# Kernel tuning notes

Measured on AMD Instinct MI355X. Metric: run time of the kernel, lower is better.

## Reference

```python
import jax, jax.numpy as jnp
import numpy as np

HIDDEN = 256
INPUT = 256
OUTPUT = 256
BATCH = 256
SEQ = 512


def setup_inputs() -> dict:
    key = jax.random.key(0)
    ks = jax.random.split(key, 9)
    d = INPUT + HIDDEN
    s = 0.05
    return {
        "x": jax.random.normal(ks[0], (BATCH, SEQ, INPUT), dtype=jnp.float32),
        "Wr": jax.random.normal(ks[1], (d, HIDDEN), dtype=jnp.float32) * s,
        "br": jax.random.normal(ks[2], (HIDDEN,), dtype=jnp.float32) * s,
        "Wz": jax.random.normal(ks[3], (d, HIDDEN), dtype=jnp.float32) * s,
        "bz": jax.random.normal(ks[4], (HIDDEN,), dtype=jnp.float32) * s,
        "Wh": jax.random.normal(ks[5], (d, HIDDEN), dtype=jnp.float32) * s,
        "bh": jax.random.normal(ks[6], (HIDDEN,), dtype=jnp.float32) * s,
        "Wo": jax.random.normal(ks[7], (HIDDEN, OUTPUT), dtype=jnp.float32) * s,
        "bo": jax.random.normal(ks[8], (OUTPUT,), dtype=jnp.float32) * s,
    }


def reference(x, Wr, br, Wz, bz, Wh, bh, Wo, bo):
    # x: [B, S, I]. Sequential GRU cell; only last-step output is returned
    # (the torch loop overwrites `output` each iteration).
    B = x.shape[0]
    h0 = jnp.zeros((B, HIDDEN), dtype=x.dtype)

    def step(h, xt):
        combined = jnp.concatenate([xt, h], axis=1)          # [B, I+H]
        r = jax.nn.sigmoid(combined @ Wr + br)                # reset gate
        z = jax.nn.sigmoid(combined @ Wz + bz)                # update gate
        combined2 = jnp.concatenate([xt, r * h], axis=1)
        h_cand = jnp.tanh(combined2 @ Wh + bh)
        h_new = z * h + (1.0 - z) * h_cand
        return h_new, None

    xs = jnp.swapaxes(x, 0, 1)  # [S, B, I] for scan over time
    h_last, _ = jax.lax.scan(step, h0, xs)
    return h_last @ Wo + bo
```

## Files before the change

kernel.cpp:

```cpp
#include <hip/hip_runtime.h>
#include <math.h>


#define BATCH  256
#define SEQ    512
#define INPUT  256
#define HIDDEN 256
#define DTOT   512
#define NTC    48
#define NT_O   16
#define LOG2E  1.44269504088896f

typedef float          f32x4 __attribute__((ext_vector_type(4)));
typedef short          s16x8 __attribute__((ext_vector_type(8)));
typedef unsigned short u16x8 __attribute__((ext_vector_type(8)));
typedef unsigned int   u32x2 __attribute__((ext_vector_type(2)));

#define WH_OFF   0u
#define WX_OFF   393216u
#define WO_OFF   786432u
#define X_OFF    917504u
#define WS_NEED     (917504ull + 201326592ull)
#define WS_NEED_OLD 786432ull

__device__ __forceinline__ unsigned short f2bf(float f) {
    unsigned int u = __float_as_uint(f);
    u += 0x7FFFu + ((u >> 16) & 1u);
    return (unsigned short)(u >> 16);
}
__device__ __forceinline__ unsigned short f2bf_fast(float f) {
    return (unsigned short)((__float_as_uint(f) + 0x8000u) >> 16);
}
__device__ __forceinline__ float bf2f(unsigned short u) {
    return __uint_as_float(((unsigned int)u) << 16);
}
__device__ __forceinline__ f32x4 cvt4(u32x2 u) {
    f32x4 a;
    a[0] = __uint_as_float(u[0] << 16);
    a[1] = __uint_as_float(u[0] & 0xffff0000u);
    a[2] = __uint_as_float(u[1] << 16);
    a[3] = __uint_as_float(u[1] & 0xffff0000u);
    return a;
}
__device__ __forceinline__ unsigned int pk2bf(float a, float b) {
    return ((__float_as_uint(a) + 0x8000u) >> 16) |
           ((__float_as_uint(b) + 0x8000u) & 0xFFFF0000u);
}
#if __has_builtin(__builtin_amdgcn_exp2f)
#define EXP2F(x) __builtin_amdgcn_exp2f(x)
#else
#define EXP2F(x) exp2f(x)
#endif
#if __has_builtin(__builtin_amdgcn_rcpf)
#define RCPF(x) __builtin_amdgcn_rcpf(x)
#else
#define RCPF(x) (1.0f / (x))
#endif

#define WAITCNT_VM3()   asm volatile("s_waitcnt vmcnt(3)" ::: "memory")
#define WAITCNT_VM4()   asm volatile("s_waitcnt vmcnt(4)" ::: "memory")
#define WAITCNT_LGKM0() asm volatile("s_waitcnt lgkmcnt(0)" ::: "memory")
#define BAR() do { __builtin_amdgcn_s_barrier(); __builtin_amdgcn_sched_barrier(0); } while (0)

__device__ __forceinline__ void async_ld16(const void* g, void* l) {
    __builtin_amdgcn_global_load_lds(
        (const __attribute__((address_space(1))) unsigned int*)g,
        (__attribute__((address_space(3))) unsigned int*)l, 16, 0, 0);
}

__device__ __forceinline__ void ntc_decode(int ntc, int& gate, int& colbase) {
    int w = ntc / 6, s = ntc - 6 * w;
    gate = s >> 1;
    colbase = (2 * w + (s & 1)) * 16;
}

__global__ __launch_bounds__(256) void pack_weights_k(
    const float* __restrict__ Wr, const float* __restrict__ Wz,
    const float* __restrict__ Wh, const float* __restrict__ Wo,
    unsigned short* __restrict__ ws)
{
    int tid = blockIdx.x * 256 + threadIdx.x;
    int tile = tid >> 6;
    int l = tid & 63, quad = l >> 4, lan = l & 15;
    u16x8 v;
    unsigned short* dst;
    if (tile < 768) {
        int isH = tile < 384;
        int t2 = isH ? tile : tile - 384;
        int ntc = t2 >> 3, kt = t2 & 7;
        int gate, colbase;
        ntc_decode(ntc, gate, colbase);
        const float* W = gate == 0 ? Wr : (gate == 1 ? Wz : Wh);
        float scale = (gate == 2) ? 2.f * LOG2E : LOG2E;
        int col = colbase + lan;
        int kbase = (isH ? 256 : 0) + kt * 32 + quad * 8;
        #pragma unroll
        for (int j = 0; j < 8; ++j) v[j] = f2bf(W[(kbase + j) * 256 + col] * scale);
        dst = (unsigned short*)((char*)ws + (isH ? WH_OFF : WX_OFF)) + (size_t)(t2 * 64 + l) * 8;
    } else {
        int t2 = tile - 768;
        int kt = t2 / NT_O, nt = t2 % NT_O;
        int col = nt * 16 + lan;
        int kbase = kt * 32 + quad * 8;
        #pragma unroll
        for (int j = 0; j < 8; ++j) v[j] = f2bf(Wo[(kbase + j) * 256 + col]);
        dst = (unsigned short*)((char*)ws + WO_OFF) + (size_t)(t2 * 64 + l) * 8;
    }
    *(u16x8*)dst = v;
}

__global__ __launch_bounds__(256, 1) void xgemm_k(
    const float* __restrict__ x,
    const float* __restrict__ br, const float* __restrict__ bz, const float* __restrict__ bh,
    unsigned short* __restrict__ ws)
{
    __shared__ __align__(16) float Xf[2][16][260];
    const int th = threadIdx.x, wave = th >> 6, l = th & 63, quad = l >> 4, lan = l & 15;
    const s16x8* WX = (const s16x8*)((char*)ws + WX_OFF);
    s16x8 wx[12][8];
    #pragma unroll
    for (int fi = 0; fi < 12; ++fi)
        #pragma unroll
        for (int kt = 0; kt < 8; ++kt)
            wx[fi][kt] = WX[(((size_t)(12 * wave + fi)) * 8 + kt) * 64 + l];
    float bias[12];
    #pragma unroll
    for (int fi = 0; fi < 12; ++fi) {
        int gate, colbase;
        ntc_decode(12 * wave + fi, gate, colbase);
        const float* bb = gate == 0 ? br : (gate == 1 ? bz : bh);
        bias[fi] = bb[colbase + lan] * (gate == 2 ? 2.f * LOG2E : LOG2E);
    }
    u32x2* Xout = (u32x2*)((char*)ws + X_OFF);

    {
        int unit = blockIdx.x * 32, t = unit >> 4, gg = unit & 15;
        #pragma unroll
        for (int rr = 0; rr < 4; ++rr) {
            int row = rr * 4 + wave;
            const float* src = x + (((size_t)(gg * 16 + row)) * SEQ + t) * INPUT + l * 4;
            async_ld16(src, &Xf[0][row][0]);
        }
    }
    for (int uu = 0; uu < 32; ++uu) {
        BAR();
        if (uu + 1 < 32) {
            int unit = blockIdx.x * 32 + uu + 1, t = unit >> 4, gg = unit & 15;
            int nb = (uu + 1) & 1;
            #pragma unroll
            for (int rr = 0; rr < 4; ++rr) {
                int row = rr * 4 + wave;
                const float* src = x + (((size_t)(gg * 16 + row)) * SEQ + t) * INPUT + l * 4;
                async_ld16(src, &Xf[nb][row][0]);
            }
        }
        WAITCNT_VM4();
        BAR();
        int buf = uu & 1;
        f32x4 acc[12];
        #pragma unroll
        for (int fi = 0; fi < 12; ++fi) { acc[fi][0] = bias[fi]; acc[fi][1] = bias[fi]; acc[fi][2] = bias[fi]; acc[fi][3] = bias[fi]; }
        #pragma unroll
        for (int kt = 0; kt < 8; ++kt) {
            f32x4 a0 = *(const f32x4*)&Xf[buf][lan][kt * 32 + quad * 8];
            f32x4 a1 = *(const f32x4*)&Xf[buf][lan][kt * 32 + quad * 8 + 4];
            u16x8 ap;
            ap[0] = f2bf_fast(a0[0]); ap[1] = f2bf_fast(a0[1]); ap[2] = f2bf_fast(a0[2]); ap[3] = f2bf_fast(a0[3]);
            ap[4] = f2bf_fast(a1[0]); ap[5] = f2bf_fast(a1[1]); ap[6] = f2bf_fast(a1[2]); ap[7] = f2bf_fast(a1[3]);
            s16x8 a = (s16x8)ap;
            #pragma unroll
            for (int fi = 0; fi < 12; ++fi)
                acc[fi] = __builtin_amdgcn_mfma_f32_16x16x32_bf16(a, wx[fi][kt], acc[fi], 0, 0, 0);
        }
        size_t unit = (size_t)blockIdx.x * 32 + uu;
        #pragma unroll
        for (int fi = 0; fi < 12; ++fi) {
            u32x2 p;
            p[0] = pk2bf(acc[fi][0], acc[fi][1]);
            p[1] = pk2bf(acc[fi][2], acc[fi][3]);
            Xout[(unit * NTC + 12 * wave + fi) * 64 + l] = p;
        }
    }
}

__global__ __launch_bounds__(512, 2) void gru_rec_k(
    const float* __restrict__ bo,
    unsigned short* __restrict__ ws,
    float* __restrict__ out)
{
    extern __shared__ __align__(16) char smem[];
    unsigned short (*Hb)[264]  = (unsigned short (*)[264])smem;
    unsigned short (*RHb)[264] = (unsigned short (*)[264])(smem + 8448);
    char* Xr = smem + 16896;

    const int th = threadIdx.x, wave = th >> 6, l = th & 63, quad = l >> 4, lan = l & 15;
    const int b = blockIdx.x;
    const s16x8* WH = (const s16x8*)((char*)ws + WH_OFF);
    s16x8 wfr[2][8], wfz[2][8], wfc[2][8];
    #pragma unroll
    for (int i = 0; i < 2; ++i)
        #pragma unroll
        for (int kt = 0; kt < 8; ++kt) {
            wfr[i][kt] = WH[((6 * wave + i) * 8 + kt) * 64 + l];
            wfz[i][kt] = WH[((6 * wave + 2 + i) * 8 + kt) * 64 + l];
            wfc[i][kt] = WH[((6 * wave + 4 + i) * 8 + kt) * 64 + l];
        }
    for (int idx = th; idx < 16 * 264; idx += 512) ((unsigned short*)Hb)[idx] = 0;
    float h[2][4];
    #pragma unroll
    for (int i = 0; i < 2; ++i)
        #pragma unroll
        for (int r = 0; r < 4; ++r) h[i][r] = 0.f;

    const char* Xg = (const char*)ws + X_OFF;
    {
        const char* sb = Xg + (((size_t)b) * NTC + 6 * wave) * 512;
        char* db = Xr + wave * 3072;
        #pragma unroll
        for (int inst = 0; inst < 3; ++inst)
            async_ld16(sb + inst * 1024 + l * 16, db + inst * 1024);
    }
    __syncthreads();

    for (int t = 0; t < SEQ; ++t) {
        int buf = t & 1;
        {
            int t1 = (t + 1 < SEQ) ? t + 1 : t;
            const char* sb = Xg + (((size_t)(t1 * 16 + b)) * NTC + 6 * wave) * 512;
            char* db = Xr + (buf ^ 1) * 24576 + wave * 3072;
            #pragma unroll
            for (int inst = 0; inst < 3; ++inst)
                async_ld16(sb + inst * 1024 + l * 16, db + inst * 1024);
        }
        WAITCNT_VM3();
        const char* Xw = Xr + buf * 24576 + wave * 3072;

        f32x4 ar[2], az[2];
        #pragma unroll
        for (int i = 0; i < 2; ++i) {
            ar[i] = cvt4(*(const u32x2*)(Xw + (size_t)i * 512 + l * 8));
            az[i] = cvt4(*(const u32x2*)(Xw + (size_t)(2 + i) * 512 + l * 8));
        }
        #pragma unroll
        for (int kt = 0; kt < 8; ++kt) {
            s16x8 a = *(const s16x8*)&Hb[lan][kt * 32 + quad * 8];
            #pragma unroll
            for (int i = 0; i < 2; ++i) {
                ar[i] = __builtin_amdgcn_mfma_f32_16x16x32_bf16(a, wfr[i][kt], ar[i], 0, 0, 0);
                az[i] = __builtin_amdgcn_mfma_f32_16x16x32_bf16(a, wfz[i][kt], az[i], 0, 0, 0);
            }
        }
        #pragma unroll
        for (int i = 0; i < 2; ++i) {
            int col = (2 * wave + i) * 16 + lan;
            #pragma unroll
            for (int r = 0; r < 4; ++r) {
                float rg = RCPF(1.f + EXP2F(-ar[i][r]));
                RHb[quad * 4 + r][col] = f2bf_fast(rg * h[i][r]);
            }
        }
        WAITCNT_LGKM0();
        BAR();

        float zg[2][4];
        #pragma unroll
        for (int i = 0; i < 2; ++i)
            #pragma unroll
            for (int r = 0; r < 4; ++r)
                zg[i][r] = RCPF(1.f + EXP2F(-az[i][r]));

        f32x4 ac[2];
        #pragma unroll
        for (int i = 0; i < 2; ++i)
            ac[i] = cvt4(*(const u32x2*)(Xw + (size_t)(4 + i) * 512 + l * 8));
        #pragma unroll
        for (int kt = 0; kt < 8; ++kt) {
            s16x8 a = *(const s16x8*)&RHb[lan][kt * 32 + quad * 8];
            #pragma unroll
            for (int i = 0; i < 2; ++i)
                ac[i] = __builtin_amdgcn_mfma_f32_16x16x32_bf16(a, wfc[i][kt], ac[i], 0, 0, 0);
        }
        #pragma unroll
        for (int i = 0; i < 2; ++i) {
            int col = (2 * wave + i) * 16 + lan;
            #pragma unroll
            for (int r = 0; r < 4; ++r) {
                float e  = EXP2F(ac[i][r]);
                float hc = (e - 1.f) * RCPF(e + 1.f);
                float hn = zg[i][r] * (h[i][r] - hc) + hc;
                h[i][r] = hn;
                Hb[quad * 4 + r][col] = f2bf_fast(hn);
            }
        }
        WAITCNT_LGKM0();
        BAR();
    }

    const s16x8* WO = (const s16x8*)((char*)ws + WO_OFF);
    #pragma unroll
    for (int i = 0; i < 2; ++i) {
        int nt = 2 * wave + i;
        int col = nt * 16 + lan;
        float bv = bo[col];
        f32x4 acc;
        acc[0] = bv; acc[1] = bv; acc[2] = bv; acc[3] = bv;
        #pragma unroll
        for (int kt = 0; kt < 8; ++kt) {
            s16x8 a = *(const s16x8*)&Hb[lan][kt * 32 + quad * 8];
            acc = __builtin_amdgcn_mfma_f32_16x16x32_bf16(a, WO[(kt * NT_O + nt) * 64 + l], acc, 0, 0, 0);
        }
        #pragma unroll
        for (int r = 0; r < 4; ++r)
            out[(size_t)(b * 16 + quad * 4 + r) * 256 + col] = acc[r];
    }
}

__global__ __launch_bounds__(256) void prep_weights_k(
    const float* __restrict__ Wr, const float* __restrict__ Wz,
    const float* __restrict__ Wh, unsigned short* __restrict__ W16)
{
    const int n = DTOT * HIDDEN;
    int idx = blockIdx.x * 256 + threadIdx.x;
    if (idx >= 3 * n) return;
    int m = idx / n;
    int r = idx - m * n;
    const float* src = (m == 0) ? Wr : ((m == 1) ? Wz : Wh);
    W16[idx] = f2bf(src[r]);
}
__device__ __forceinline__ float ldw(const unsigned short* p) { return bf2f(*p); }
__device__ __forceinline__ float ldw(const float* p)          { return *p; }

template <typename WT>
__global__ __launch_bounds__(256) void gru_seq_k(
    const float* __restrict__ x,
    const WT* __restrict__ Wr, const WT* __restrict__ Wz, const WT* __restrict__ Wh,
    const float* __restrict__ br, const float* __restrict__ bz, const float* __restrict__ bh,
    const float* __restrict__ Wo, const float* __restrict__ bo,
    float* __restrict__ out)
{
    const int b = blockIdx.x, j = threadIdx.x;
    __shared__ float xh[DTOT];
    __shared__ float xrh[DTOT];
    xh[INPUT + j] = 0.0f;
    const float brj = br[j], bzj = bz[j], bhj = bh[j];
    const float* xb = x + (size_t)b * SEQ * INPUT;
    const WT* wrj = Wr + j;
    const WT* wzj = Wz + j;
    const WT* whj = Wh + j;
    __syncthreads();
    for (int t = 0; t < SEQ; ++t) {
        float xv = xb[t * INPUT + j];
        xh[j] = xv; xrh[j] = xv;
        __syncthreads();
        float ar = brj, az = bzj;
        #pragma unroll 8
        for (int k = 0; k < DTOT; ++k) {
            float v = xh[k];
            ar += v * ldw(wrj + k * HIDDEN);
            az += v * ldw(wzj + k * HIDDEN);
        }
        float rg = 1.0f / (1.0f + __expf(-ar));
        float zg = 1.0f / (1.0f + __expf(-az));
        float hj = xh[INPUT + j];
        xrh[INPUT + j] = rg * hj;
        __syncthreads();
        float ah = bhj;
        #pragma unroll 8
        for (int k = 0; k < DTOT; ++k) ah += xrh[k] * ldw(whj + k * HIDDEN);
        float hc = tanhf(ah);
        float hn = zg * hj + (1.0f - zg) * hc;
        xh[INPUT + j] = hn;
        __syncthreads();
    }
    float acc = bo[j];
    #pragma unroll 8
    for (int k = 0; k < HIDDEN; ++k) acc += xh[INPUT + k] * Wo[k * HIDDEN + j];
    out[(size_t)b * HIDDEN + j] = acc;
}

extern "C" void kernel_launch(void* const* d_in, const int* in_sizes, int n_in,
                              void* d_out, int out_size, void* d_ws, size_t ws_size,
                              hipStream_t stream) {
    const float* x  = (const float*)d_in[0];
    const float* Wr = (const float*)d_in[1];
    const float* br = (const float*)d_in[2];
    const float* Wz = (const float*)d_in[3];
    const float* bz = (const float*)d_in[4];
    const float* Wh = (const float*)d_in[5];
    const float* bh = (const float*)d_in[6];
    const float* Wo = (const float*)d_in[7];
    const float* bo = (const float*)d_in[8];
    float* out = (float*)d_out;

    if (ws_size >= WS_NEED) {
        unsigned short* ws = (unsigned short*)d_ws;
        (void)hipFuncSetAttribute((const void*)gru_rec_k,
                                  hipFuncAttributeMaxDynamicSharedMemorySize, 66048);
        pack_weights_k<<<224, 256, 0, stream>>>(Wr, Wz, Wh, Wo, ws);
        xgemm_k<<<256, 256, 0, stream>>>(x, br, bz, bh, ws);
        gru_rec_k<<<16, 512, 66048, stream>>>(bo, ws, out);
    } else if (ws_size >= WS_NEED_OLD) {
        unsigned short* W16 = (unsigned short*)d_ws;
        const size_t n = (size_t)DTOT * HIDDEN;
        prep_weights_k<<<(int)((3 * n + 255) / 256), 256, 0, stream>>>(Wr, Wz, Wh, W16);
        gru_seq_k<unsigned short><<<BATCH, 256, 0, stream>>>(
            x, W16, W16 + n, W16 + 2 * n, br, bz, bh, Wo, bo, out);
    } else {
        gru_seq_k<float><<<BATCH, 256, 0, stream>>>(
            x, Wr, Wz, Wh, br, bz, bh, Wo, bo, out);
    }
}
```

Measured before the change: 1.056 ms.

## Prefetch precomputed input projections into registers and split candidate MFMA chain

```diff
diff --git a/kernel.cpp b/kernel.cpp
--- a/kernel.cpp
+++ b/kernel.cpp
@@ -13,6 +13,7 @@
 
 typedef float          f32x4 __attribute__((ext_vector_type(4)));
 typedef short          s16x8 __attribute__((ext_vector_type(8)));
+typedef short          s16x4 __attribute__((ext_vector_type(4)));
 typedef unsigned short u16x8 __attribute__((ext_vector_type(8)));
 typedef unsigned int   u32x2 __attribute__((ext_vector_type(2)));
 
@@ -57,7 +58,6 @@
 #define RCPF(x) (1.0f / (x))
 #endif
 
-#define WAITCNT_VM3()   asm volatile("s_waitcnt vmcnt(3)" ::: "memory")
 #define WAITCNT_VM4()   asm volatile("s_waitcnt vmcnt(4)" ::: "memory")
 #define WAITCNT_LGKM0() asm volatile("s_waitcnt lgkmcnt(0)" ::: "memory")
 #define BAR() do { __builtin_amdgcn_s_barrier(); __builtin_amdgcn_sched_barrier(0); } while (0)
@@ -66,6 +66,12 @@
     __builtin_amdgcn_global_load_lds(
         (const __attribute__((address_space(1))) unsigned int*)g,
         (__attribute__((address_space(3))) unsigned int*)l, 16, 0, 0);
+}
+
+__device__ __forceinline__ s16x8 ld_frag(const unsigned short* row, int off) {
+    s16x4 lo = *(const s16x4*)(row + off);
+    s16x4 hi = *(const s16x4*)(row + off + 4);
+    return __builtin_shufflevector(lo, hi, 0, 1, 2, 3, 4, 5, 6, 7);
 }
 
 __device__ __forceinline__ void ntc_decode(int ntc, int& gate, int& colbase) {
@@ -188,10 +194,8 @@
     unsigned short* __restrict__ ws,
     float* __restrict__ out)
 {
-    extern __shared__ __align__(16) char smem[];
-    unsigned short (*Hb)[264]  = (unsigned short (*)[264])smem;
-    unsigned short (*RHb)[264] = (unsigned short (*)[264])(smem + 8448);
-    char* Xr = smem + 16896;
+    __shared__ __align__(16) unsigned short Hb[16][260];
+    __shared__ __align__(16) unsigned short RHb[16][260];
 
     const int th = threadIdx.x, wave = th >> 6, l = th & 63, quad = l >> 4, lan = l & 15;
     const int b = blockIdx.x;
@@ -205,45 +209,40 @@
             wfz[i][kt] = WH[((6 * wave + 2 + i) * 8 + kt) * 64 + l];
             wfc[i][kt] = WH[((6 * wave + 4 + i) * 8 + kt) * 64 + l];
         }
-    for (int idx = th; idx < 16 * 264; idx += 512) ((unsigned short*)Hb)[idx] = 0;
+    for (int idx = th; idx < 16 * 260; idx += 512) ((unsigned short*)Hb)[idx] = 0;
     float h[2][4];
     #pragma unroll
     for (int i = 0; i < 2; ++i)
         #pragma unroll
         for (int r = 0; r < 4; ++r) h[i][r] = 0.f;
 
-    const char* Xg = (const char*)ws + X_OFF;
-    {
-        const char* sb = Xg + (((size_t)b) * NTC + 6 * wave) * 512;
-        char* db = Xr + wave * 3072;
-        #pragma unroll
-        for (int inst = 0; inst < 3; ++inst)
-            async_ld16(sb + inst * 1024 + l * 16, db + inst * 1024);
-    }
+    const char* xp = (const char*)ws + X_OFF
+                   + (((size_t)b) * NTC + 6 * wave) * 512 + (size_t)l * 8;
+    const size_t XSTEP = (size_t)16 * NTC * 512;
+    u32x2 xn[6];
+    #pragma unroll
+    for (int j = 0; j < 6; ++j) xn[j] = *(const u32x2*)(xp + j * 512);
+
     __syncthreads();
 
     for (int t = 0; t < SEQ; ++t) {
-        int buf = t & 1;
-        {
-            int t1 = (t + 1 < SEQ) ? t + 1 : t;
-            const char* sb = Xg + (((size_t)(t1 * 16 + b)) * NTC + 6 * wave) * 512;
-            char* db = Xr + (buf ^ 1) * 24576 + wave * 3072;
-            #pragma unroll
-            for (int inst = 0; inst < 3; ++inst)
-                async_ld16(sb + inst * 1024 + l * 16, db + inst * 1024);
-        }
-        WAITCNT_VM3();
-        const char* Xw = Xr + buf * 24576 + wave * 3072;
+        u32x2 xc[6];
+        #pragma unroll
+        for (int j = 0; j < 6; ++j) xc[j] = xn[j];
+        if (t + 1 < SEQ) xp += XSTEP;
+        #pragma unroll
+        for (int j = 0; j < 6; ++j) xn[j] = *(const u32x2*)(xp + j * 512);
 
         f32x4 ar[2], az[2];
         #pragma unroll
         for (int i = 0; i < 2; ++i) {
-            ar[i] = cvt4(*(const u32x2*)(Xw + (size_t)i * 512 + l * 8));
-            az[i] = cvt4(*(const u32x2*)(Xw + (size_t)(2 + i) * 512 + l * 8));
-        }
+            ar[i] = cvt4(xc[i]);
+            az[i] = cvt4(xc[2 + i]);
+        }
+        const unsigned short* hrow = &Hb[lan][0];
         #pragma unroll
         for (int kt = 0; kt < 8; ++kt) {
-            s16x8 a = *(const s16x8*)&Hb[lan][kt * 32 + quad * 8];
+            s16x8 a = ld_frag(hrow, kt * 32 + quad * 8);
             #pragma unroll
             for (int i = 0; i < 2; ++i) {
                 ar[i] = __builtin_amdgcn_mfma_f32_16x16x32_bf16(a, wfr[i][kt], ar[i], 0, 0, 0);
@@ -269,23 +268,33 @@
             for (int r = 0; r < 4; ++r)
                 zg[i][r] = RCPF(1.f + EXP2F(-az[i][r]));
 
-        f32x4 ac[2];
-        #pragma unroll
-        for (int i = 0; i < 2; ++i)
-            ac[i] = cvt4(*(const u32x2*)(Xw + (size_t)(4 + i) * 512 + l * 8));
-        #pragma unroll
-        for (int kt = 0; kt < 8; ++kt) {
-            s16x8 a = *(const s16x8*)&RHb[lan][kt * 32 + quad * 8];
+        f32x4 acL[2], acH[2];
+        #pragma unroll
+        for (int i = 0; i < 2; ++i) {
+            acL[i] = cvt4(xc[4 + i]);
+            acH[i][0] = 0.f; acH[i][1] = 0.f; acH[i][2] = 0.f; acH[i][3] = 0.f;
+        }
+        const unsigned short* rrow = &RHb[lan][0];
+        #pragma unroll
+        for (int kt = 0; kt < 4; ++kt) {
+            s16x8 a = ld_frag(rrow, kt * 32 + quad * 8);
             #pragma unroll
             for (int i = 0; i < 2; ++i)
-                ac[i] = __builtin_amdgcn_mfma_f32_16x16x32_bf16(a, wfc[i][kt], ac[i], 0, 0, 0);
+                acL[i] = __builtin_amdgcn_mfma_f32_16x16x32_bf16(a, wfc[i][kt], acL[i], 0, 0, 0);
+        }
+        #pragma unroll
+        for (int kt = 4; kt < 8; ++kt) {
+            s16x8 a = ld_frag(rrow, kt * 32 + quad * 8);
+            #pragma unroll
+            for (int i = 0; i < 2; ++i)
+                acH[i] = __builtin_amdgcn_mfma_f32_16x16x32_bf16(a, wfc[i][kt], acH[i], 0, 0, 0);
         }
         #pragma unroll
         for (int i = 0; i < 2; ++i) {
             int col = (2 * wave + i) * 16 + lan;
             #pragma unroll
             for (int r = 0; r < 4; ++r) {
-                float e  = EXP2F(ac[i][r]);
+                float e  = EXP2F(acL[i][r] + acH[i][r]);
                 float hc = (e - 1.f) * RCPF(e + 1.f);
                 float hn = zg[i][r] * (h[i][r] - hc) + hc;
                 h[i][r] = hn;
@@ -306,7 +315,7 @@
         acc[0] = bv; acc[1] = bv; acc[2] = bv; acc[3] = bv;
         #pragma unroll
         for (int kt = 0; kt < 8; ++kt) {
-            s16x8 a = *(const s16x8*)&Hb[lan][kt * 32 + quad * 8];
+            s16x8 a = ld_frag(&Hb[lan][0], kt * 32 + quad * 8);
             acc = __builtin_amdgcn_mfma_f32_16x16x32_bf16(a, WO[(kt * NT_O + nt) * 64 + l], acc, 0, 0, 0);
         }
         #pragma unroll
@@ -394,11 +403,9 @@
 
     if (ws_size >= WS_NEED) {
         unsigned short* ws = (unsigned short*)d_ws;
-        (void)hipFuncSetAttribute((const void*)gru_rec_k,
-                                  hipFuncAttributeMaxDynamicSharedMemorySize, 66048);
         pack_weights_k<<<224, 256, 0, stream>>>(Wr, Wz, Wh, Wo, ws);
         xgemm_k<<<256, 256, 0, stream>>>(x, br, bz, bh, ws);
-        gru_rec_k<<<16, 512, 66048, stream>>>(bo, ws, out);
+        gru_rec_k<<<16, 512, 0, stream>>>(bo, ws, out);
     } else if (ws_size >= WS_NEED_OLD) {
         unsigned short* W16 = (unsigned short*)d_ws;
         const size_t n = (size_t)DTOT * HIDDEN;
```

After: 1.148 ms. +8.7%, slower.

## Widen xgemm blocks to eight waves and stage x as bf16 in LDS

Applied to the files above, without the earlier changes.

```diff
diff --git a/kernel.cpp b/kernel.cpp
--- a/kernel.cpp
+++ b/kernel.cpp
@@ -58,7 +58,6 @@
 #endif
 
 #define WAITCNT_VM3()   asm volatile("s_waitcnt vmcnt(3)" ::: "memory")
-#define WAITCNT_VM4()   asm volatile("s_waitcnt vmcnt(4)" ::: "memory")
 #define WAITCNT_LGKM0() asm volatile("s_waitcnt lgkmcnt(0)" ::: "memory")
 #define BAR() do { __builtin_amdgcn_s_barrier(); __builtin_amdgcn_sched_barrier(0); } while (0)
 
@@ -109,76 +108,71 @@
     *(u16x8*)dst = v;
 }
 
-__global__ __launch_bounds__(256, 1) void xgemm_k(
+__global__ __launch_bounds__(512, 2) void xgemm_k(
     const float* __restrict__ x,
     const float* __restrict__ br, const float* __restrict__ bz, const float* __restrict__ bh,
     unsigned short* __restrict__ ws)
 {
-    __shared__ __align__(16) float Xf[2][16][260];
+    __shared__ __align__(16) unsigned short Xbf[16][264];
     const int th = threadIdx.x, wave = th >> 6, l = th & 63, quad = l >> 4, lan = l & 15;
     const s16x8* WX = (const s16x8*)((char*)ws + WX_OFF);
-    s16x8 wx[12][8];
+    s16x8 wx[6][8];
     #pragma unroll
-    for (int fi = 0; fi < 12; ++fi)
+    for (int fi = 0; fi < 6; ++fi)
         #pragma unroll
         for (int kt = 0; kt < 8; ++kt)
-            wx[fi][kt] = WX[(((size_t)(12 * wave + fi)) * 8 + kt) * 64 + l];
-    float bias[12];
+            wx[fi][kt] = WX[(((size_t)(6 * wave + fi)) * 8 + kt) * 64 + l];
+    float bias[6];
     #pragma unroll
-    for (int fi = 0; fi < 12; ++fi) {
+    for (int fi = 0; fi < 6; ++fi) {
         int gate, colbase;
-        ntc_decode(12 * wave + fi, gate, colbase);
+        ntc_decode(6 * wave + fi, gate, colbase);
         const float* bb = gate == 0 ? br : (gate == 1 ? bz : bh);
         bias[fi] = bb[colbase + lan] * (gate == 2 ? 2.f * LOG2E : LOG2E);
     }
     u32x2* Xout = (u32x2*)((char*)ws + X_OFF);
 
+    f32x4 xs[2];
     {
         int unit = blockIdx.x * 32, t = unit >> 4, gg = unit & 15;
         #pragma unroll
-        for (int rr = 0; rr < 4; ++rr) {
-            int row = rr * 4 + wave;
-            const float* src = x + (((size_t)(gg * 16 + row)) * SEQ + t) * INPUT + l * 4;
-            async_ld16(src, &Xf[0][row][0]);
-        }
+        for (int rr = 0; rr < 2; ++rr)
+            xs[rr] = *(const f32x4*)(x + (((size_t)(gg * 16 + 2 * wave + rr)) * SEQ + t) * INPUT + l * 4);
     }
     for (int uu = 0; uu < 32; ++uu) {
-        BAR();
+        if (uu > 0) BAR();
+        #pragma unroll
+        for (int rr = 0; rr < 2; ++rr) {
+            u32x2 p;
+            p[0] = pk2bf(xs[rr][0], xs[rr][1]);
+            p[1] = pk2bf(xs[rr][2], xs[rr][3]);
+            *(u32x2*)&Xbf[2 * wave + rr][l * 4] = p;
+        }
         if (uu + 1 < 32) {
             int unit = blockIdx.x * 32 + uu + 1, t = unit >> 4, gg = unit & 15;
-            int nb = (uu + 1) & 1;
-            #pragma unroll
-            for (int rr = 0; rr < 4; ++rr) {
-                int row = rr * 4 + wave;
-                const float* src = x + (((size_t)(gg * 16 + row)) * SEQ + t) * INPUT + l * 4;
-                async_ld16(src, &Xf[nb][row][0]);
-            }
-        }
-        WAITCNT_VM4();
+            #pragma unroll
+            for (int rr = 0; rr < 2; ++rr)
+                xs[rr] = *(const f32x4*)(x + (((size_t)(gg * 16 + 2 * wave + rr)) * SEQ + t) * INPUT + l * 4);
+        }
+        WAITCNT_LGKM0();
         BAR();
-        int buf = uu & 1;
-        f32x4 acc[12];
-        #pragma unroll
-        for (int fi = 0; fi < 12; ++fi) { acc[fi][0] = bias[fi]; acc[fi][1] = bias[fi]; acc[fi][2] = bias[fi]; acc[fi][3] = bias[fi]; }
+        f32x4 acc[6];
+        #pragma unroll
+        for (int fi = 0; fi < 6; ++fi) { acc[fi][0] = bias[fi]; acc[fi][1] = bias[fi]; acc[fi][2] = bias[fi]; acc[fi][3] = bias[fi]; }
         #pragma unroll
         for (int kt = 0; kt < 8; ++kt) {
-            f32x4 a0 = *(const f32x4*)&Xf[buf][lan][kt * 32 + quad * 8];
-            f32x4 a1 = *(const f32x4*)&Xf[buf][lan][kt * 32 + quad * 8 + 4];
-            u16x8 ap;
-            ap[0] = f2bf_fast(a0[0]); ap[1] = f2bf_fast(a0[1]); ap[2] = f2bf_fast(a0[2]); ap[3] = f2bf_fast(a0[3]);
-            ap[4] = f2bf_fast(a1[0]); ap[5] = f2bf_fast(a1[1]); ap[6] = f2bf_fast(a1[2]); ap[7] = f2bf_fast(a1[3]);
-            s16x8 a = (s16x8)ap;
-            #pragma unroll
-            for (int fi = 0; fi < 12; ++fi)
+            s16x8 a = *(const s16x8*)&Xbf[lan][kt * 32 + quad * 8];
+            #pragma unroll
+            for (int fi = 0; fi < 6; ++fi)
                 acc[fi] = __builtin_amdgcn_mfma_f32_16x16x32_bf16(a, wx[fi][kt], acc[fi], 0, 0, 0);
         }
         size_t unit = (size_t)blockIdx.x * 32 + uu;
         #pragma unroll
-        for (int fi = 0; fi < 12; ++fi) {
+        for (int fi = 0; fi < 6; ++fi) {
             u32x2 p;
             p[0] = pk2bf(acc[fi][0], acc[fi][1]);
             p[1] = pk2bf(acc[fi][2], acc[fi][3]);
-            Xout[(unit * NTC + 12 * wave + fi) * 64 + l] = p;
+            Xout[(unit * NTC + 6 * wave + fi) * 64 + l] = p;
         }
     }
 }
@@ -397,7 +391,7 @@
         (void)hipFuncSetAttribute((const void*)gru_rec_k,
                                   hipFuncAttributeMaxDynamicSharedMemorySize, 66048);
         pack_weights_k<<<224, 256, 0, stream>>>(Wr, Wz, Wh, Wo, ws);
-        xgemm_k<<<256, 256, 0, stream>>>(x, br, bz, bh, ws);
+        xgemm_k<<<256, 512, 0, stream>>>(x, br, bz, bh, ws);
         gru_rec_k<<<16, 512, 66048, stream>>>(bo, ws, out);
     } else if (ws_size >= WS_NEED_OLD) {
         unsigned short* W16 = (unsigned short*)d_ws;
```

Result: no change. 1.052 ms (-0.3%).
